# Kernel optimization log

Hardware: AMD Instinct MI355X
Metric: run time of the kernel (lower is better)

The kernel has to match this reference:

```python
import jax, jax.numpy as jnp
import numpy as np

B, S, D = 4, 2048, 1024
H, HD = 16, 64
WINDOW = 128


def setup_inputs() -> dict:
    key = jax.random.key(0)
    ks = jax.random.split(key, 8)
    scale = 1.0 / np.sqrt(D)
    return {
        "hidden_states": jax.random.normal(ks[0], (B, S, D), dtype=jnp.float32),
        "attention_mask": jnp.zeros((B, 1, 1, S), dtype=jnp.float32),
        "Wq": jax.random.normal(ks[1], (D, D), dtype=jnp.float32) * scale,
        "bq": jnp.zeros((D,), dtype=jnp.float32),
        "Wk": jax.random.normal(ks[2], (D, D), dtype=jnp.float32) * scale,
        "bk": jnp.zeros((D,), dtype=jnp.float32),
        "Wv": jax.random.normal(ks[3], (D, D), dtype=jnp.float32) * scale,
        "bv": jnp.zeros((D,), dtype=jnp.float32),
    }


def _proj(x, W, b):
    # [b t D] -> [b h t d]
    p = x @ W.T + b
    return p.reshape(x.shape[0], x.shape[1], H, HD).transpose(0, 2, 1, 3)


def reference(hidden_states, attention_mask, Wq, bq, Wk, bk, Wv, bv):
    q = _proj(hidden_states, Wq, bq)  # [b h t d]
    k = _proj(hidden_states, Wk, bk)
    v = _proj(hidden_states, Wv, bv)

    scores = jnp.einsum("bhtd,bhsd->bhts", q, k) / np.sqrt(HD)  # [b h t s]
    pos = jnp.arange(S)
    i, j = pos[:, None], pos[None, :]
    # causal (j <= i) AND sliding window (i - j <= w)
    allowed = (j <= i) & ((i - j) <= WINDOW)  # [t s]
    scores = jnp.where(allowed[None, None], scores, -jnp.inf)
    scores = scores + attention_mask  # additive padding mask [b,1,1,s]
    probs = jax.nn.softmax(scores, axis=-1)  # dropout identity in eval
    ctx = jnp.einsum("bhts,bhsd->bhtd", probs, v)
    return ctx.transpose(0, 2, 1, 3).reshape(B, S, D)
```

## Files before the change

kernel.cpp:

```cpp
#include <hip/hip_runtime.h>
#include <cstdint>

#define BDIM 4
#define SEQ 2048
#define DMODEL 1024
#define NH 16
#define HDIM 64

typedef __attribute__((ext_vector_type(8))) short bf16x8;
typedef __attribute__((ext_vector_type(4))) float f32x4;
typedef __attribute__((ext_vector_type(4))) int i32x4;
typedef __attribute__((ext_vector_type(4))) unsigned short u16x4;

#define MFMA16(a, b, c) __builtin_amdgcn_mfma_f32_16x16x32_bf16(a, b, c, 0, 0, 0)

__device__ __forceinline__ unsigned short f2bf(float x) {
    unsigned int u = __float_as_uint(x);
    unsigned int r = (u + 0x7FFFu + ((u >> 16) & 1u)) >> 16;
    return (unsigned short)r;
}

__device__ __forceinline__ void gload16(const void* g, void* l) {
    __builtin_amdgcn_global_load_lds(
        (const __attribute__((address_space(1))) unsigned int*)g,
        (__attribute__((address_space(3))) unsigned int*)l, 16, 0, 0);
}

__global__ __launch_bounds__(256) void k_cvt_x(const float* __restrict__ src,
                                               unsigned short* __restrict__ dst) {
    int i = blockIdx.x * 256 + threadIdx.x;
    float4 v = ((const float4*)src)[i];
    u16x4 o = {f2bf(v.x), f2bf(v.y), f2bf(v.z), f2bf(v.w)};
    ((u16x4*)dst)[i] = o;
}

__global__ __launch_bounds__(256) void k_cvt_w(const float* __restrict__ wq,
                                               const float* __restrict__ wk,
                                               const float* __restrict__ wv,
                                               unsigned short* __restrict__ dst) {
    int i = blockIdx.x * 256 + threadIdx.x;
    int e = i << 2;
    int which = e >> 20;
    int off = e & 0xFFFFF;
    const float* s = which == 0 ? wq : (which == 1 ? wk : wv);
    float4 v = *(const float4*)(s + off);
    u16x4 o = {f2bf(v.x), f2bf(v.y), f2bf(v.z), f2bf(v.w)};
    ((u16x4*)dst)[i] = o;
}

__global__ __launch_bounds__(512, 2)
void k_qkv(const unsigned short* __restrict__ X,
           const unsigned short* __restrict__ W,
           const float* __restrict__ bq,
           const float* __restrict__ bk,
           const float* __restrict__ bv,
           unsigned short* __restrict__ Qo,
           unsigned short* __restrict__ Ko,
           unsigned short* __restrict__ Vt) {
    __shared__ unsigned short ldsA[4][256 * 32];
    __shared__ unsigned short ldsB[4][128 * 32];
    const int tid = threadIdx.x;
    const int lane = tid & 63, wid = tid >> 6;
    const int wm = wid >> 1, wn = wid & 1;
    const int l15 = lane & 15, g = lane >> 4;
    const int bid0 = blockIdx.x;
    const int bid = (bid0 & 7) * 96 + (bid0 >> 3);
    const int bx = bid % 24, by = bid / 24;
    const int m0 = by * 256, n0 = bx * 128;

#define STAGE_A(d, kt)                                                      \
    {                                                                       \
        _Pragma("unroll") for (int i = 0; i < 2; ++i) {                     \
            const int e = i * 512 + tid;                                    \
            const int row = e >> 2, sl = e & 3;                             \
            const int slx = sl ^ ((row >> 1) & 3);                          \
            gload16(X + (size_t)(m0 + row) * DMODEL + (kt) * 32 + slx * 8,  \
                    (char*)&ldsA[d][0] + e * 16);                           \
        }                                                                   \
    }
#define STAGE_B(d, kt)                                                      \
    {                                                                       \
        const int e = tid;                                                  \
        const int row = e >> 2, sl = e & 3;                                 \
        const int slx = sl ^ ((row >> 1) & 3);                              \
        gload16(W + (size_t)(n0 + row) * DMODEL + (kt) * 32 + slx * 8,      \
                (char*)&ldsB[d][0] + e * 16);                               \
    }

    f32x4 acc[4][4];
#pragma unroll
    for (int i = 0; i < 4; ++i)
#pragma unroll
        for (int j = 0; j < 4; ++j) acc[i][j] = (f32x4){0.f, 0.f, 0.f, 0.f};

    STAGE_A(0, 0); STAGE_B(0, 0);
    STAGE_A(1, 1); STAGE_B(1, 1);
    STAGE_A(2, 2); STAGE_B(2, 2);
    asm volatile("s_waitcnt vmcnt(6)" ::: "memory");
    __builtin_amdgcn_s_barrier();

    const int ar = wm * 64 + l15;
    const int br = wn * 64 + l15;

#pragma unroll 4
    for (int t = 0; t < 32; ++t) {
        const int cb = t & 3;
        bf16x8 av[4], bvv[4];
#pragma unroll
        for (int mf = 0; mf < 4; ++mf) {
            const int row = ar + mf * 16;
            av[mf] = *(const bf16x8*)((const char*)&ldsA[cb][0] +
                      ((row * 64 + g * 16) ^ (((row >> 1) & 3) << 4)));
        }
#pragma unroll
        for (int nf = 0; nf < 4; ++nf) {
            const int row = br + nf * 16;
            bvv[nf] = *(const bf16x8*)((const char*)&ldsB[cb][0] +
                       ((row * 64 + g * 16) ^ (((row >> 1) & 3) << 4)));
        }
        if (t < 29) { STAGE_A((t + 3) & 3, t + 3); STAGE_B((t + 3) & 3, t + 3); }
        asm volatile("s_waitcnt lgkmcnt(0)" ::: "memory");
        __builtin_amdgcn_sched_barrier(0);
        __builtin_amdgcn_s_setprio(1);
#pragma unroll
        for (int mf = 0; mf < 4; ++mf)
#pragma unroll
            for (int nf = 0; nf < 4; ++nf)
                acc[mf][nf] = MFMA16(av[mf], bvv[nf], acc[mf][nf]);
        __builtin_amdgcn_s_setprio(0);
        if (t < 29)      { asm volatile("s_waitcnt vmcnt(6)" ::: "memory"); }
        else if (t == 29){ asm volatile("s_waitcnt vmcnt(3)" ::: "memory"); }
        else if (t == 30){ asm volatile("s_waitcnt vmcnt(0)" ::: "memory"); }
        __builtin_amdgcn_s_barrier();
    }
#undef STAGE_A
#undef STAGE_B

    const int bb = m0 >> 11;
    const int sbase = (m0 & 2047) + wm * 64 + g * 4;
#pragma unroll
    for (int nf = 0; nf < 4; ++nf) {
        const int col = n0 + wn * 64 + nf * 16 + l15;
        const int proj = col >> 10, rem = col & 1023;
        const int h = rem >> 6, hd = rem & 63;
        const float bias = (proj == 0 ? bq : proj == 1 ? bk : bv)[rem];
        const float scl = (proj == 0) ? 0.125f : 1.0f;
        unsigned short* dstp = (proj == 0 ? Qo : proj == 1 ? Ko : Vt) +
                               (size_t)(bb * NH + h) * (SEQ * HDIM) +
                               (proj == 2 ? (size_t)hd * SEQ : (size_t)hd);
        const int stride = (proj == 2) ? 1 : HDIM;
#pragma unroll
        for (int mf = 0; mf < 4; ++mf) {
            const int s0 = sbase + mf * 16;
#pragma unroll
            for (int r = 0; r < 4; ++r)
                dstp[(size_t)(s0 + r) * stride] = f2bf((acc[mf][nf][r] + bias) * scl);
        }
    }
}

__global__ __launch_bounds__(256) void k_attn(const unsigned short* __restrict__ Qg,
                                              const unsigned short* __restrict__ Kg,
                                              const unsigned short* __restrict__ Vtg,
                                              const float* __restrict__ amask,
                                              float* __restrict__ out) {
    __shared__ unsigned short kl[224 * 64];
    __shared__ unsigned short vl[64 * 224];
    __shared__ unsigned short pl[4 * 16 * 160];
    const int bid0 = blockIdx.x;
    const int bid = (bid0 & 7) * 256 + (bid0 >> 3);
    const int bh = bid >> 5, qb = bid & 31;
    const int b = bh >> 4, h = bh & 15;
    const int q0 = qb << 6;
    const int kstart = q0 - 144;
    const int tid = threadIdx.x, lane = tid & 63, w = tid >> 6;
    const int l15 = lane & 15, g = lane >> 4;

#pragma unroll
    for (int it = 0; it < 7; ++it) {
        const int c = it * 256 + tid;
        {
            const int row = c >> 3, sl = c & 7;
            const int key = kstart + row;
            i32x4 v = {0, 0, 0, 0};
            if ((unsigned)key < (unsigned)SEQ)
                v = *(const i32x4*)(Kg + (size_t)(bh * SEQ + key) * HDIM + sl * 8);
            *(i32x4*)((char*)kl + ((row * 128 + sl * 16) ^ ((row & 7) << 4))) = v;
        }
        {
            const int row = c / 28, sl = c - row * 28;
            const int key0 = kstart + sl * 8;
            i32x4 v = {0, 0, 0, 0};
            if ((unsigned)key0 < (unsigned)SEQ)
                v = *(const i32x4*)(Vtg + (size_t)(bh * HDIM + row) * SEQ + key0);
            *(i32x4*)((char*)vl + ((row * 448 + sl * 16) ^ ((row & 7) << 4))) = v;
        }
    }
    const int iq = q0 + w * 16 + l15;
    const bf16x8 qf0 = *(const bf16x8*)(Qg + (size_t)(bh * SEQ + iq) * HDIM + g * 8);
    const bf16x8 qf1 = *(const bf16x8*)(Qg + (size_t)(bh * SEQ + iq) * HDIM + 32 + g * 8);
    __syncthreads();

    char* pbase = (char*)pl + w * 5120;
    const int swq = (l15 & 7) << 4;
    float s[40];

    __builtin_amdgcn_s_setprio(1);
#pragma unroll
    for (int t = 0; t < 5; ++t) {
        const int tloc = w * 16 + t * 32;
        bf16x8 kf[2][2];
#pragma unroll
        for (int m = 0; m < 2; ++m) {
            const int row = tloc + m * 16 + l15;
            const int swz = (row & 7) << 4;
            kf[m][0] = *(const bf16x8*)((const char*)kl + ((row * 128 + g * 16) ^ swz));
            kf[m][1] = *(const bf16x8*)((const char*)kl + ((row * 128 + 64 + g * 16) ^ swz));
        }
        f32x4 sa0 = {0.f, 0.f, 0.f, 0.f}, sa1 = {0.f, 0.f, 0.f, 0.f};
        sa0 = MFMA16(kf[0][0], qf0, sa0);
        sa0 = MFMA16(kf[0][1], qf1, sa0);
        sa1 = MFMA16(kf[1][0], qf0, sa1);
        sa1 = MFMA16(kf[1][1], qf1, sa1);
#pragma unroll
        for (int f = 0; f < 2; ++f) {
            const int jb = kstart + tloc + f * 16 + g * 4;
            float4 m4 = {0.f, 0.f, 0.f, 0.f};
            if ((unsigned)jb < (unsigned)SEQ) m4 = *(const float4*)(amask + b * SEQ + jb);
            const float mvv[4] = {m4.x, m4.y, m4.z, m4.w};
#pragma unroll
            for (int r = 0; r < 4; ++r) {
                const int jg = jb + r;
                const float sc = (f == 0 ? sa0[r] : sa1[r]) + mvv[r];
                const bool ok = (jg >= 0) && (jg <= iq) && (iq - jg <= 128);
                s[t * 8 + f * 4 + r] = ok ? sc : -3.0e38f;
            }
        }
    }
    __builtin_amdgcn_s_setprio(0);

    float tr[20];
#pragma unroll
    for (int i = 0; i < 20; ++i) tr[i] = fmaxf(s[i], s[i + 20]);
#pragma unroll
    for (int i = 0; i < 10; ++i) tr[i] = fmaxf(tr[i], tr[i + 10]);
#pragma unroll
    for (int i = 0; i < 5; ++i) tr[i] = fmaxf(tr[i], tr[i + 5]);
    float m = fmaxf(fmaxf(tr[0], tr[1]), fmaxf(tr[2], fmaxf(tr[3], tr[4])));
    m = fmaxf(m, __shfl_xor(m, 16));
    m = fmaxf(m, __shfl_xor(m, 32));

    float ls0 = 0.f, ls1 = 0.f, ls2 = 0.f, ls3 = 0.f;
#pragma unroll
    for (int i = 0; i < 40; i += 4) {
        float p0 = exp2f((s[i + 0] - m) * 1.44269504f);
        float p1 = exp2f((s[i + 1] - m) * 1.44269504f);
        float p2 = exp2f((s[i + 2] - m) * 1.44269504f);
        float p3 = exp2f((s[i + 3] - m) * 1.44269504f);
        s[i + 0] = p0; s[i + 1] = p1; s[i + 2] = p2; s[i + 3] = p3;
        ls0 += p0; ls1 += p1; ls2 += p2; ls3 += p3;
    }
    float l = (ls0 + ls1) + (ls2 + ls3);
    l += __shfl_xor(l, 16);
    l += __shfl_xor(l, 32);

#pragma unroll
    for (int t = 0; t < 5; ++t) {
#pragma unroll
        for (int f = 0; f < 2; ++f) {
            u16x4 pu = {f2bf(s[t * 8 + f * 4 + 0]), f2bf(s[t * 8 + f * 4 + 1]),
                        f2bf(s[t * 8 + f * 4 + 2]), f2bf(s[t * 8 + f * 4 + 3])};
            *(u16x4*)(pbase + ((l15 * 320 + t * 64 + f * 32 + g * 8) ^ swq)) = pu;
        }
    }
    asm volatile("s_waitcnt lgkmcnt(0)" ::: "memory");
    __builtin_amdgcn_sched_barrier(0);

    f32x4 acc[4];
#pragma unroll
    for (int i = 0; i < 4; ++i) acc[i] = (f32x4){0.f, 0.f, 0.f, 0.f};
    __builtin_amdgcn_s_setprio(1);
#pragma unroll
    for (int t = 0; t < 5; ++t) {
        const int tloc = w * 16 + t * 32;
        const bf16x8 pf = *(const bf16x8*)(pbase + ((l15 * 320 + t * 64 + g * 16) ^ swq));
#pragma unroll
        for (int fn = 0; fn < 4; ++fn) {
            const int vrow = fn * 16 + l15;
            const bf16x8 vf = *(const bf16x8*)((const char*)vl +
                ((vrow * 448 + tloc * 2 + g * 16) ^ ((vrow & 7) << 4)));
            acc[fn] = MFMA16(pf, vf, acc[fn]);
        }
    }
    __builtin_amdgcn_s_setprio(0);

    float linv[4];
#pragma unroll
    for (int r = 0; r < 4; ++r) linv[r] = 1.0f / __shfl(l, g * 4 + r);
#pragma unroll
    for (int fn = 0; fn < 4; ++fn) {
#pragma unroll
        for (int r = 0; r < 4; ++r) {
            const int qrow = q0 + w * 16 + g * 4 + r;
            out[(size_t)(b * SEQ + qrow) * DMODEL + h * HDIM + fn * 16 + l15] =
                acc[fn][r] * linv[r];
        }
    }
}

extern "C" void kernel_launch(void* const* d_in, const int* in_sizes, int n_in,
                              void* d_out, int out_size, void* d_ws, size_t ws_size,
                              hipStream_t stream) {
    const float* hs = (const float*)d_in[0];
    const float* amask = (const float*)d_in[1];
    const float* wq = (const float*)d_in[2];
    const float* bq = (const float*)d_in[3];
    const float* wk = (const float*)d_in[4];
    const float* bk = (const float*)d_in[5];
    const float* wv = (const float*)d_in[6];
    const float* bv = (const float*)d_in[7];
    float* out = (float*)d_out;

    char* p = (char*)d_ws;
    unsigned short* Xbf = (unsigned short*)p;
    unsigned short* Wbf = (unsigned short*)(p + 16777216);
    unsigned short* Vtb = (unsigned short*)(p + 16777216 + 6291456);
    unsigned short* Qb = Vtb + 8388608;
    unsigned short* Kb = Qb + 8388608;

    k_cvt_x<<<8192, 256, 0, stream>>>(hs, Xbf);
    k_cvt_w<<<3072, 256, 0, stream>>>(wq, wk, wv, Wbf);
    k_qkv<<<768, 512, 0, stream>>>(Xbf, Wbf, bq, bk, bv, Qb, Kb, Vtb);
    k_attn<<<2048, 256, 0, stream>>>(Qb, Kb, Vtb, amask, out);
}
```

Baseline: 141.3 us.

## Shrink QKV GEMM tile to 128x128 with double-buffered LDS pipeline

Cuts the QKV projection GEMM block tile from 256x128 (512 threads, 4-stage LDS ring) to 128x128 (256 threads, 2-stage double buffer). Grid size doubles, blocks use less LDS, and the swizzle and launch configuration are updated to match. The goal is more resident blocks per CU and better load balance across the grid. In exchange there is less reuse of B per block and a shallower prefetch: each step waits with vmcnt(0), which can leave global load latency exposed.

```diff
diff --git a/kernel.cpp b/kernel.cpp
--- a/kernel.cpp
+++ b/kernel.cpp
@@ -48,7 +48,7 @@
     ((u16x4*)dst)[i] = o;
 }
 
-__global__ __launch_bounds__(512, 2)
+__global__ __launch_bounds__(256) __attribute__((amdgpu_waves_per_eu(4)))
 void k_qkv(const unsigned short* __restrict__ X,
            const unsigned short* __restrict__ W,
            const float* __restrict__ bq,
@@ -57,35 +57,29 @@
            unsigned short* __restrict__ Qo,
            unsigned short* __restrict__ Ko,
            unsigned short* __restrict__ Vt) {
-    __shared__ unsigned short ldsA[4][256 * 32];
-    __shared__ unsigned short ldsB[4][128 * 32];
+    __shared__ unsigned short ldsA[2][128 * 32];
+    __shared__ unsigned short ldsB[2][128 * 32];
     const int tid = threadIdx.x;
     const int lane = tid & 63, wid = tid >> 6;
     const int wm = wid >> 1, wn = wid & 1;
     const int l15 = lane & 15, g = lane >> 4;
     const int bid0 = blockIdx.x;
-    const int bid = (bid0 & 7) * 96 + (bid0 >> 3);
+    const int bid = (bid0 & 7) * 192 + (bid0 >> 3);
     const int bx = bid % 24, by = bid / 24;
-    const int m0 = by * 256, n0 = bx * 128;
-
-#define STAGE_A(d, kt)                                                      \
+    const int m0 = by * 128, n0 = bx * 128;
+
+#define STAGE(d, kt)                                                        \
     {                                                                       \
         _Pragma("unroll") for (int i = 0; i < 2; ++i) {                     \
-            const int e = i * 512 + tid;                                    \
+            const int e = i * 256 + tid;                                    \
             const int row = e >> 2, sl = e & 3;                             \
             const int slx = sl ^ ((row >> 1) & 3);                          \
             gload16(X + (size_t)(m0 + row) * DMODEL + (kt) * 32 + slx * 8,  \
                     (char*)&ldsA[d][0] + e * 16);                           \
+            gload16(W + (size_t)(n0 + row) * DMODEL + (kt) * 32 + slx * 8,  \
+                    (char*)&ldsB[d][0] + e * 16);                           \
         }                                                                   \
     }
-#define STAGE_B(d, kt)                                                      \
-    {                                                                       \
-        const int e = tid;                                                  \
-        const int row = e >> 2, sl = e & 3;                                 \
-        const int slx = sl ^ ((row >> 1) & 3);                              \
-        gload16(W + (size_t)(n0 + row) * DMODEL + (kt) * 32 + slx * 8,      \
-                (char*)&ldsB[d][0] + e * 16);                               \
-    }
 
     f32x4 acc[4][4];
 #pragma unroll
@@ -93,32 +87,29 @@
 #pragma unroll
         for (int j = 0; j < 4; ++j) acc[i][j] = (f32x4){0.f, 0.f, 0.f, 0.f};
 
-    STAGE_A(0, 0); STAGE_B(0, 0);
-    STAGE_A(1, 1); STAGE_B(1, 1);
-    STAGE_A(2, 2); STAGE_B(2, 2);
-    asm volatile("s_waitcnt vmcnt(6)" ::: "memory");
+    STAGE(0, 0);
+    asm volatile("s_waitcnt vmcnt(0)" ::: "memory");
     __builtin_amdgcn_s_barrier();
 
     const int ar = wm * 64 + l15;
     const int br = wn * 64 + l15;
 
-#pragma unroll 4
+#pragma unroll 2
     for (int t = 0; t < 32; ++t) {
-        const int cb = t & 3;
+        const char* Ac = (const char*)&ldsA[t & 1][0];
+        const char* Bc = (const char*)&ldsB[t & 1][0];
+        if (t < 31) STAGE((t + 1) & 1, t + 1);
         bf16x8 av[4], bvv[4];
 #pragma unroll
         for (int mf = 0; mf < 4; ++mf) {
             const int row = ar + mf * 16;
-            av[mf] = *(const bf16x8*)((const char*)&ldsA[cb][0] +
-                      ((row * 64 + g * 16) ^ (((row >> 1) & 3) << 4)));
+            av[mf] = *(const bf16x8*)(Ac + ((row * 64 + g * 16) ^ ((((row) >> 1) & 3) << 4)));
         }
 #pragma unroll
         for (int nf = 0; nf < 4; ++nf) {
             const int row = br + nf * 16;
-            bvv[nf] = *(const bf16x8*)((const char*)&ldsB[cb][0] +
-                       ((row * 64 + g * 16) ^ (((row >> 1) & 3) << 4)));
-        }
-        if (t < 29) { STAGE_A((t + 3) & 3, t + 3); STAGE_B((t + 3) & 3, t + 3); }
+            bvv[nf] = *(const bf16x8*)(Bc + ((row * 64 + g * 16) ^ ((((row) >> 1) & 3) << 4)));
+        }
         asm volatile("s_waitcnt lgkmcnt(0)" ::: "memory");
         __builtin_amdgcn_sched_barrier(0);
         __builtin_amdgcn_s_setprio(1);
@@ -128,13 +119,10 @@
             for (int nf = 0; nf < 4; ++nf)
                 acc[mf][nf] = MFMA16(av[mf], bvv[nf], acc[mf][nf]);
         __builtin_amdgcn_s_setprio(0);
-        if (t < 29)      { asm volatile("s_waitcnt vmcnt(6)" ::: "memory"); }
-        else if (t == 29){ asm volatile("s_waitcnt vmcnt(3)" ::: "memory"); }
-        else if (t == 30){ asm volatile("s_waitcnt vmcnt(0)" ::: "memory"); }
+        if (t < 31) { asm volatile("s_waitcnt vmcnt(0)" ::: "memory"); }
         __builtin_amdgcn_s_barrier();
     }
-#undef STAGE_A
-#undef STAGE_B
+#undef STAGE
 
     const int bb = m0 >> 11;
     const int sbase = (m0 & 2047) + wm * 64 + g * 4;
@@ -330,6 +318,6 @@
 
     k_cvt_x<<<8192, 256, 0, stream>>>(hs, Xbf);
     k_cvt_w<<<3072, 256, 0, stream>>>(wq, wk, wv, Wbf);
-    k_qkv<<<768, 512, 0, stream>>>(Xbf, Wbf, bq, bk, bv, Qb, Kb, Vtb);
+    k_qkv<<<1536, 256, 0, stream>>>(Xbf, Wbf, bq, bk, bv, Qb, Kb, Vtb);
     k_attn<<<2048, 256, 0, stream>>>(Qb, Kb, Vtb, amask, out);
 }
```

After: 153.0 us. 8.3% more time.
